# Optimization experiments

Measured on AMD Instinct MI355X. Metric: run time of the kernel, lower is better.

The kernel has to match this reference:

```python
import jax, jax.numpy as jnp
import numpy as np

B, T, C, H = 8, 2048, 1024, 64

def setup_inputs() -> dict:
    key = jax.random.key(0)
    kx, kq, kk, kv = jax.random.split(key, 4)
    scale = 1.0 / np.sqrt(C)
    return {
        "x": jax.random.normal(kx, (B, T, C), dtype=jnp.float32),
        "Wq": jax.random.normal(kq, (C, H), dtype=jnp.float32) * scale,
        "Wk": jax.random.normal(kk, (C, H), dtype=jnp.float32) * scale,
        "Wv": jax.random.normal(kv, (C, H), dtype=jnp.float32) * scale,
    }

def reference(x, Wq, Wk, Wv):
    # q,k,v: [B,T,H]
    q = jnp.einsum('btc,ch->bth', x, Wq)
    k = jnp.einsum('btc,ch->bth', x, Wk)
    v = jnp.einsum('btc,ch->bth', x, Wv)
    scale = k.shape[-1] ** -0.5
    wei = jnp.einsum('bth,bsh->bts', q, k) * scale  # [B,T,T]
    causal = jnp.tril(jnp.ones((x.shape[1], x.shape[1]), dtype=bool))
    wei = jnp.where(causal, wei, -jnp.inf)
    wei = jax.nn.softmax(wei, axis=-1)
    out = jnp.einsum('bts,bsh->bth', wei, v)  # [B,T,H]
    return out
```

## Files before the change

### kernel.cpp

```cpp
#include <hip/hip_runtime.h>

#define B_ 8
#define T_ 2048
#define C_ 1024
#define H_ 64

typedef __bf16 bf16x8 __attribute__((ext_vector_type(8)));
typedef float  f32x4  __attribute__((ext_vector_type(4)));
typedef unsigned short u16x8 __attribute__((ext_vector_type(8)));

__device__ __forceinline__ unsigned short f2bf(float f) {
    unsigned u = __builtin_bit_cast(unsigned, f);
    u += 0x8000u;
    return (unsigned short)(u >> 16);
}

__device__ __forceinline__ float bf2f(unsigned short v) {
    unsigned u = ((unsigned)v) << 16;
    return __builtin_bit_cast(float, u);
}

__device__ __forceinline__ unsigned pack2(float lo, float hi) {
    unsigned a = __builtin_bit_cast(unsigned, lo) + 0x8000u;
    unsigned b = __builtin_bit_cast(unsigned, hi) + 0x8000u;
    return (a >> 16) | (b & 0xffff0000u);
}

union U8 { unsigned u32[4]; u16x8 v; };

__device__ __forceinline__ u16x8 cvt8(float4 f0, float4 f1) {
    U8 r;
    r.u32[0] = pack2(f0.x, f0.y);
    r.u32[1] = pack2(f0.z, f0.w);
    r.u32[2] = pack2(f1.x, f1.y);
    r.u32[3] = pack2(f1.z, f1.w);
    return r.v;
}

__device__ __forceinline__ bf16x8 load8_bf(const unsigned short* p) {
    return __builtin_bit_cast(bf16x8, *(const u16x8*)p);
}

__device__ __forceinline__ void gload_lds16(const float* g, float* l) {
    __builtin_amdgcn_global_load_lds(
        (const __attribute__((address_space(1))) unsigned int*)g,
        (__attribute__((address_space(3))) unsigned int*)l, 16, 0, 0);
}


__global__ void cast_weights(const float* __restrict__ Wq,
                             const float* __restrict__ Wk,
                             const float* __restrict__ Wv,
                             unsigned short* __restrict__ Wtf) {
    int idx = blockIdx.x * blockDim.x + threadIdx.x;
    int n   = idx % 192;
    int c   = idx / 192;
    int w   = n >> 6;
    int h   = n & 63;
    const float* W = (w == 0) ? Wq : (w == 1) ? Wk : Wv;
    int nt = n >> 4, l16 = n & 15;
    int kk = c >> 5, quad = (c >> 3) & 3, j = c & 7;
    Wtf[(size_t)(nt * 32 + kk) * 512 + l16 * 32 + quad * 8 + j] =
        f2bf(W[(size_t)c * H_ + h]);
}

__global__ __launch_bounds__(256, 2) void qkv_proj(
        const float* __restrict__ x,
        const unsigned short* __restrict__ Wtf,
        unsigned short* __restrict__ Qf,
        unsigned short* __restrict__ Kf,
        unsigned short* __restrict__ Vf) {
    __shared__ __attribute__((aligned(16))) float Axs[16 * 1024];

    const int tid  = threadIdx.x;
    const int ns   = tid >> 6;
    const int lane = tid & 63;
    const int l16  = lane & 15;
    const int quad = lane >> 4;
    const size_t r0 = (size_t)blockIdx.x * 16;
    const int bb     = (int)(r0 >> 11);
    const int tloc0  = (int)(r0 & (T_ - 1));
    const int t16_0  = tloc0 >> 4;
    const int s32    = tloc0 >> 5;
    const int half16 = t16_0 & 1;

#pragma unroll
    for (int jj = 0; jj < 16; jj++) {
        int j   = ns * 16 + jj;
        int row = j >> 2;
        int S0  = (j & 3) * 64;
        int g   = (S0 + lane) ^ (row & 7);
        const float* gp = x + (r0 + row) * C_ + g * 4;
        float* lp = &Axs[row * 1024 + S0 * 4];
        gload_lds16(gp, lp);
    }

    f32x4 acc[3];
#pragma unroll
    for (int i = 0; i < 3; i++) acc[i] = (f32x4){0.f, 0.f, 0.f, 0.f};

    const int xsw = l16 & 7;
    const unsigned short* wp = Wtf + (size_t)(ns * 3 * 32) * 512
                               + l16 * 32 + quad * 8;
    const float* Arow = &Axs[l16 * 1024];

    __syncthreads();

#pragma unroll 4
    for (int kk = 0; kk < 32; kk++) {
        int g0 = kk * 8 + quad * 2;
        float4 f0 = *(const float4*)(Arow + (size_t)((g0    ) ^ xsw) * 4);
        float4 f1 = *(const float4*)(Arow + (size_t)((g0 + 1) ^ xsw) * 4);
        bf16x8 a0 = __builtin_bit_cast(bf16x8, cvt8(f0, f1));
#pragma unroll
        for (int i = 0; i < 3; i++) {
            bf16x8 b = load8_bf(wp + (size_t)(i * 32 + kk) * 512);
            acc[i] = __builtin_amdgcn_mfma_f32_16x16x32_bf16(a0, b, acc[i], 0, 0, 0);
        }
    }

    __syncthreads();
    unsigned short* E = (unsigned short*)Axs;
#pragma unroll
    for (int i = 0; i < 3; i++) {
        int nt = ns * 3 + i;
#pragma unroll
        for (int r = 0; r < 4; r++) {
            unsigned short bv = f2bf(acc[i][r]);
            int off;
            if (nt < 4) {
                off = (nt >> 1) * 512 + (quad * 4 + r) * 32 +
                      ((nt & 1) * 2 + (l16 >> 3)) * 8 + (l16 & 7);
            } else if (nt < 8) {
                int nk = nt - 4;
                off = 1024 + (nk >> 1) * 512 + (quad * 4 + r) * 32 +
                      ((nk & 1) * 2 + (l16 >> 3)) * 8 + (l16 & 7);
            } else {
                int ht = nt - 8;
                off = 2048 + ht * 256 + l16 * 16 + quad * 4 + r;
            }
            E[off] = bv;
        }
    }
    __syncthreads();

    {
        int ch = tid >> 6;
        int g  = tid & 63;
        unsigned short* dst = (ch < 2) ? Qf : Kf;
        int part = ch & 1;
        dst += ((size_t)(bb * 128 + t16_0) * 2 + part) * 512;
        *(u16x8*)(dst + g * 8) = *(const u16x8*)(&E[ch * 512 + g * 8]);
    }
    if (tid < 128) {
        int ht   = tid >> 5;
        int rr   = tid & 31;
        int l16v = rr >> 1;
        int hh   = rr & 1;
        unsigned short* dst = Vf + ((size_t)(bb * 64 + s32) * 4 + ht) * 512
                              + l16v * 32 + half16 * 16 + hh * 8;
        *(u16x8*)dst = *(const u16x8*)(&E[2048 + ht * 256 + l16v * 16 + hh * 8]);
    }
}

#define PROW 33
#define OMS2 66

__global__ __launch_bounds__(256) void attn(
        const unsigned short* __restrict__ Qf,
        const unsigned short* __restrict__ Kf,
        const unsigned short* __restrict__ Vf,
        float* __restrict__ out) {
    __shared__ unsigned int ps_[4 * 32 * PROW];
    __shared__ unsigned short Om_[4 * 32 * OMS2];
    __shared__ float mred_[4][32];
    __shared__ float lred_[4][32];

    const int tid  = threadIdx.x;
    const int wave = tid >> 6;
    const int lane = tid & 63;
    const int l16  = lane & 15;
    const int quad = lane >> 4;
    const int b    = blockIdx.x & 7;
    const int qt32 = blockIdx.x >> 3;
    const int q0   = qt32 * 32;
    const int tdiag = qt32 >> 1;

    const int loff = l16 * 32 + quad * 8;

    bf16x8 qf[2][2];
#pragma unroll
    for (int qg = 0; qg < 2; qg++) {
        const unsigned short* Qfb = Qf + (size_t)((b * 128 + qt32 * 2 + qg) * 2) * 512;
        qf[qg][0] = load8_bf(Qfb + loff);
        qf[qg][1] = load8_bf(Qfb + 512 + loff);
    }

    f32x4 o[8];
#pragma unroll
    for (int i = 0; i < 8; i++) o[i] = (f32x4){0.f, 0.f, 0.f, 0.f};
    float m_run[2] = {-1e30f, -1e30f}, l_run[2] = {0.f, 0.f};

    const float scale = 0.125f;
    const unsigned short* Kfb = Kf + (size_t)b * 128 * 1024;
    const unsigned short* Vfb = Vf + (size_t)b * 64 * 2048;
    unsigned int* Pw = &ps_[wave * 32 * PROW];

    for (int t = wave; t <= tdiag; t += 4) {
        bf16x8 vf[8];
#pragma unroll
        for (int ks = 0; ks < 2; ks++)
#pragma unroll
            for (int ht = 0; ht < 4; ht++)
                vf[ht * 2 + ks] = load8_bf(
                    Vfb + ((size_t)(t * 2 + ks) * 4 + ht) * 512 + loff);

        f32x4 s[2][4];
#pragma unroll
        for (int nt = 0; nt < 4; nt++) {
            const unsigned short* kp = Kfb + (size_t)(t * 4 + nt) * 1024;
            bf16x8 kf0 = load8_bf(kp + loff);
            bf16x8 kf1 = load8_bf(kp + 512 + loff);
#pragma unroll
            for (int qg = 0; qg < 2; qg++) {
                f32x4 z = (f32x4){0.f, 0.f, 0.f, 0.f};
                z = __builtin_amdgcn_mfma_f32_16x16x32_bf16(kf0, qf[qg][0], z, 0, 0, 0);
                z = __builtin_amdgcn_mfma_f32_16x16x32_bf16(kf1, qf[qg][1], z, 0, 0, 0);
                s[qg][nt] = z;
            }
        }

#pragma unroll
        for (int qg = 0; qg < 2; qg++)
#pragma unroll
            for (int nt = 0; nt < 4; nt++)
#pragma unroll
                for (int r = 0; r < 4; r++) s[qg][nt][r] *= scale;

        if (t == tdiag) {
#pragma unroll
            for (int qg = 0; qg < 2; qg++) {
                int q = q0 + qg * 16 + l16;
#pragma unroll
                for (int nt = 0; nt < 4; nt++)
#pragma unroll
                    for (int r = 0; r < 4; r++) {
                        int key = t * 64 + nt * 16 + quad * 4 + r;
                        if (key > q) s[qg][nt][r] = -1e30f;
                    }
            }
        }

#pragma unroll
        for (int qg = 0; qg < 2; qg++) {
            float m0 = fmaxf(fmaxf(s[qg][0][0], s[qg][0][1]), fmaxf(s[qg][0][2], s[qg][0][3]));
            float m1 = fmaxf(fmaxf(s[qg][1][0], s[qg][1][1]), fmaxf(s[qg][1][2], s[qg][1][3]));
            float m2 = fmaxf(fmaxf(s[qg][2][0], s[qg][2][1]), fmaxf(s[qg][2][2], s[qg][2][3]));
            float m3 = fmaxf(fmaxf(s[qg][3][0], s[qg][3][1]), fmaxf(s[qg][3][2], s[qg][3][3]));
            float mx = fmaxf(fmaxf(m0, m1), fmaxf(m2, m3));
            mx = fmaxf(mx, __shfl_xor(mx, 16));
            mx = fmaxf(mx, __shfl_xor(mx, 32));
            const float m_new = fmaxf(m_run[qg], mx);
            const float alpha = __expf(m_run[qg] - m_new);
            m_run[qg] = m_new;

            float rs = 0.f;
#pragma unroll
            for (int nt = 0; nt < 4; nt++) {
#pragma unroll
                for (int i = 0; i < 2; i++) {
                    float p0 = __expf(s[qg][nt][2 * i]     - m_new);
                    float p1 = __expf(s[qg][nt][2 * i + 1] - m_new);
                    rs += p0 + p1;
                    Pw[(qg * 16 + l16) * PROW + nt * 8 + quad * 2 + i] = pack2(p0, p1);
                }
            }
            rs += __shfl_xor(rs, 16);
            rs += __shfl_xor(rs, 32);
            l_run[qg] = l_run[qg] * alpha + rs;

#pragma unroll
            for (int ht = 0; ht < 4; ht++)
#pragma unroll
                for (int r = 0; r < 4; r++) o[qg * 4 + ht][r] *= alpha;
        }

#pragma unroll
        for (int ks = 0; ks < 2; ks++) {
#pragma unroll
            for (int qg = 0; qg < 2; qg++) {
                bf16x8 pB = __builtin_bit_cast(bf16x8,
                    *(const u16x8*)(&Pw[(qg * 16 + l16) * PROW + ks * 16 + quad * 4]));
#pragma unroll
                for (int ht = 0; ht < 4; ht++)
                    o[qg * 4 + ht] = __builtin_amdgcn_mfma_f32_16x16x32_bf16(
                        vf[ht * 2 + ks], pB, o[qg * 4 + ht], 0, 0, 0);
            }
        }
    }

#pragma unroll
    for (int qg = 0; qg < 2; qg++) {
#pragma unroll
        for (int ht = 0; ht < 4; ht++)
#pragma unroll
            for (int r = 0; r < 4; r++)
                Om_[(wave * 32 + qg * 16 + l16) * OMS2 + ht * 16 + quad * 4 + r] =
                    f2bf(o[qg * 4 + ht][r]);
        if (quad == 0) {
            mred_[wave][qg * 16 + l16] = m_run[qg];
            lred_[wave][qg * 16 + l16] = l_run[qg];
        }
    }
    __syncthreads();

    const int hcol = tid & 63;
    const int qr0  = tid >> 6;
#pragma unroll
    for (int qq = 0; qq < 8; qq++) {
        const int q = qr0 + qq * 4;
        float M = -1e30f;
#pragma unroll
        for (int w = 0; w < 4; w++) M = fmaxf(M, mred_[w][q]);
        float lt = 0.f, ov = 0.f;
#pragma unroll
        for (int w = 0; w < 4; w++) {
            float e = __expf(mred_[w][q] - M);
            lt += e * lred_[w][q];
            ov += e * bf2f(Om_[(w * 32 + q) * OMS2 + hcol]);
        }
        out[((size_t)b * T_ + q0 + q) * H_ + hcol] = ov / lt;
    }
}

extern "C" void kernel_launch(void* const* d_in, const int* in_sizes, int n_in,
                              void* d_out, int out_size, void* d_ws, size_t ws_size,
                              hipStream_t stream) {
    const float* x  = (const float*)d_in[0];
    const float* Wq = (const float*)d_in[1];
    const float* Wk = (const float*)d_in[2];
    const float* Wv = (const float*)d_in[3];
    float* out = (float*)d_out;

    unsigned short* Qf  = (unsigned short*)d_ws;
    unsigned short* Kf  = Qf + (size_t)B_ * T_ * H_;
    unsigned short* Vf  = Kf + (size_t)B_ * T_ * H_;
    unsigned short* Wtf = Vf + (size_t)B_ * T_ * H_;

    cast_weights<<<(192 * C_) / 256, 256, 0, stream>>>(Wq, Wk, Wv, Wtf);
    qkv_proj<<<B_ * T_ / 16, 256, 0, stream>>>(x, Wtf, Qf, Kf, Vf);
    attn<<<B_ * (T_ / 32), 256, 0, stream>>>(Qf, Kf, Vf, out);
}
```

Measured before the change: 138.1 us.

## Make qkv_proj persistent over four row tiles with double-buffered LDS staging

Each qkv_proj block now processes 64 rows as four 16-row tiles, double-buffering the x tile in LDS. The next tile's async global-to-LDS loads are issued mid-way through the current tile's MFMA loop, so load latency overlaps compute instead of being exposed once per block. The block count drops fourfold and LDS use roughly doubles, so occupancy falls to one block per CU. That reduces the parallelism available to hide latency, and the grid of 256 blocks is small.

```diff
diff --git a/kernel.cpp b/kernel.cpp
--- a/kernel.cpp
+++ b/kernel.cpp
@@ -45,6 +45,21 @@
     __builtin_amdgcn_global_load_lds(
         (const __attribute__((address_space(1))) unsigned int*)g,
         (__attribute__((address_space(3))) unsigned int*)l, 16, 0, 0);
+}
+
+__device__ __forceinline__ void stage_rows(const float* __restrict__ x,
+                                           float* lbuf, size_t rbase,
+                                           int ns, int lane, int half) {
+#pragma unroll
+    for (int q = 0; q < 8; q++) {
+        int jj  = half * 8 + q;
+        int j   = ns * 16 + jj;
+        int row = j >> 2;
+        int S0  = (j & 3) * 64;
+        int g   = (S0 + lane) ^ (row & 7);
+        gload_lds16(x + (rbase + row) * C_ + (size_t)g * 4,
+                    lbuf + row * 1024 + S0 * 4);
+    }
 }
 
 
@@ -64,102 +79,105 @@
         f2bf(W[(size_t)c * H_ + h]);
 }
 
-__global__ __launch_bounds__(256, 2) void qkv_proj(
+__global__ __launch_bounds__(256, 1) void qkv_proj(
         const float* __restrict__ x,
         const unsigned short* __restrict__ Wtf,
         unsigned short* __restrict__ Qf,
         unsigned short* __restrict__ Kf,
         unsigned short* __restrict__ Vf) {
-    __shared__ __attribute__((aligned(16))) float Axs[16 * 1024];
+    __shared__ __attribute__((aligned(16))) float Axs[2][16 * 1024];
+    __shared__ __attribute__((aligned(16))) unsigned short E[3072];
 
     const int tid  = threadIdx.x;
     const int ns   = tid >> 6;
     const int lane = tid & 63;
     const int l16  = lane & 15;
     const int quad = lane >> 4;
-    const size_t r0 = (size_t)blockIdx.x * 16;
-    const int bb     = (int)(r0 >> 11);
-    const int tloc0  = (int)(r0 & (T_ - 1));
-    const int t16_0  = tloc0 >> 4;
-    const int s32    = tloc0 >> 5;
-    const int half16 = t16_0 & 1;
-
-#pragma unroll
-    for (int jj = 0; jj < 16; jj++) {
-        int j   = ns * 16 + jj;
-        int row = j >> 2;
-        int S0  = (j & 3) * 64;
-        int g   = (S0 + lane) ^ (row & 7);
-        const float* gp = x + (r0 + row) * C_ + g * 4;
-        float* lp = &Axs[row * 1024 + S0 * 4];
-        gload_lds16(gp, lp);
-    }
-
-    f32x4 acc[3];
-#pragma unroll
-    for (int i = 0; i < 3; i++) acc[i] = (f32x4){0.f, 0.f, 0.f, 0.f};
-
-    const int xsw = l16 & 7;
+    const size_t rblk = (size_t)blockIdx.x * 64;
+    const int bb   = (int)(rblk >> 11);
+    const int xsw  = l16 & 7;
     const unsigned short* wp = Wtf + (size_t)(ns * 3 * 32) * 512
                                + l16 * 32 + quad * 8;
-    const float* Arow = &Axs[l16 * 1024];
-
+
+    stage_rows(x, Axs[0], rblk, ns, lane, 0);
+    stage_rows(x, Axs[0], rblk, ns, lane, 1);
     __syncthreads();
 
-#pragma unroll 4
-    for (int kk = 0; kk < 32; kk++) {
-        int g0 = kk * 8 + quad * 2;
-        float4 f0 = *(const float4*)(Arow + (size_t)((g0    ) ^ xsw) * 4);
-        float4 f1 = *(const float4*)(Arow + (size_t)((g0 + 1) ^ xsw) * 4);
-        bf16x8 a0 = __builtin_bit_cast(bf16x8, cvt8(f0, f1));
+    for (int t = 0; t < 4; t++) {
+        const float* Arow = &Axs[t & 1][l16 * 1024];
+        float* bufN = &Axs[(t + 1) & 1][0];
+        const size_t rnext = rblk + (size_t)(t + 1) * 16;
+
+        f32x4 acc[3];
+#pragma unroll
+        for (int i = 0; i < 3; i++) acc[i] = (f32x4){0.f, 0.f, 0.f, 0.f};
+
+#pragma unroll
+        for (int kc = 0; kc < 4; kc++) {
+            if (kc == 1 && t < 3) stage_rows(x, bufN, rnext, ns, lane, 0);
+            if (kc == 2 && t < 3) stage_rows(x, bufN, rnext, ns, lane, 1);
+#pragma unroll
+            for (int k8 = 0; k8 < 8; k8++) {
+                const int kk = kc * 8 + k8;
+                int g0 = kk * 8 + quad * 2;
+                float4 f0 = *(const float4*)(Arow + (size_t)((g0    ) ^ xsw) * 4);
+                float4 f1 = *(const float4*)(Arow + (size_t)((g0 + 1) ^ xsw) * 4);
+                bf16x8 a0 = __builtin_bit_cast(bf16x8, cvt8(f0, f1));
+#pragma unroll
+                for (int i = 0; i < 3; i++) {
+                    bf16x8 b = load8_bf(wp + (size_t)(i * 32 + kk) * 512);
+                    acc[i] = __builtin_amdgcn_mfma_f32_16x16x32_bf16(a0, b, acc[i], 0, 0, 0);
+                }
+            }
+        }
+
+        __syncthreads();
+
+        const int tloc0  = (int)((rblk + (size_t)t * 16) & (T_ - 1));
+        const int t16_0  = tloc0 >> 4;
+        const int s32    = tloc0 >> 5;
+        const int half16 = t16_0 & 1;
+
 #pragma unroll
         for (int i = 0; i < 3; i++) {
-            bf16x8 b = load8_bf(wp + (size_t)(i * 32 + kk) * 512);
-            acc[i] = __builtin_amdgcn_mfma_f32_16x16x32_bf16(a0, b, acc[i], 0, 0, 0);
-        }
-    }
-
-    __syncthreads();
-    unsigned short* E = (unsigned short*)Axs;
-#pragma unroll
-    for (int i = 0; i < 3; i++) {
-        int nt = ns * 3 + i;
-#pragma unroll
-        for (int r = 0; r < 4; r++) {
-            unsigned short bv = f2bf(acc[i][r]);
-            int off;
-            if (nt < 4) {
-                off = (nt >> 1) * 512 + (quad * 4 + r) * 32 +
-                      ((nt & 1) * 2 + (l16 >> 3)) * 8 + (l16 & 7);
-            } else if (nt < 8) {
-                int nk = nt - 4;
-                off = 1024 + (nk >> 1) * 512 + (quad * 4 + r) * 32 +
-                      ((nk & 1) * 2 + (l16 >> 3)) * 8 + (l16 & 7);
-            } else {
-                int ht = nt - 8;
-                off = 2048 + ht * 256 + l16 * 16 + quad * 4 + r;
-            }
-            E[off] = bv;
-        }
-    }
-    __syncthreads();
-
-    {
-        int ch = tid >> 6;
-        int g  = tid & 63;
-        unsigned short* dst = (ch < 2) ? Qf : Kf;
-        int part = ch & 1;
-        dst += ((size_t)(bb * 128 + t16_0) * 2 + part) * 512;
-        *(u16x8*)(dst + g * 8) = *(const u16x8*)(&E[ch * 512 + g * 8]);
-    }
-    if (tid < 128) {
-        int ht   = tid >> 5;
-        int rr   = tid & 31;
-        int l16v = rr >> 1;
-        int hh   = rr & 1;
-        unsigned short* dst = Vf + ((size_t)(bb * 64 + s32) * 4 + ht) * 512
-                              + l16v * 32 + half16 * 16 + hh * 8;
-        *(u16x8*)dst = *(const u16x8*)(&E[2048 + ht * 256 + l16v * 16 + hh * 8]);
+            int nt = ns * 3 + i;
+#pragma unroll
+            for (int r = 0; r < 4; r++) {
+                unsigned short bv = f2bf(acc[i][r]);
+                int off;
+                if (nt < 4) {
+                    off = (nt >> 1) * 512 + (quad * 4 + r) * 32 +
+                          ((nt & 1) * 2 + (l16 >> 3)) * 8 + (l16 & 7);
+                } else if (nt < 8) {
+                    int nk = nt - 4;
+                    off = 1024 + (nk >> 1) * 512 + (quad * 4 + r) * 32 +
+                          ((nk & 1) * 2 + (l16 >> 3)) * 8 + (l16 & 7);
+                } else {
+                    int ht = nt - 8;
+                    off = 2048 + ht * 256 + l16 * 16 + quad * 4 + r;
+                }
+                E[off] = bv;
+            }
+        }
+        __syncthreads();
+
+        {
+            int ch = tid >> 6;
+            int g  = tid & 63;
+            unsigned short* dst = (ch < 2) ? Qf : Kf;
+            int part = ch & 1;
+            dst += ((size_t)(bb * 128 + t16_0) * 2 + part) * 512;
+            *(u16x8*)(dst + g * 8) = *(const u16x8*)(&E[ch * 512 + g * 8]);
+        }
+        if (tid < 128) {
+            int ht   = tid >> 5;
+            int rr   = tid & 31;
+            int l16v = rr >> 1;
+            int hh   = rr & 1;
+            unsigned short* dst = Vf + ((size_t)(bb * 64 + s32) * 4 + ht) * 512
+                                  + l16v * 32 + half16 * 16 + hh * 8;
+            *(u16x8*)dst = *(const u16x8*)(&E[2048 + ht * 256 + l16v * 16 + hh * 8]);
+        }
     }
 }
 
@@ -348,6 +366,6 @@
     unsigned short* Wtf = Vf + (size_t)B_ * T_ * H_;
 
     cast_weights<<<(192 * C_) / 256, 256, 0, stream>>>(Wq, Wk, Wv, Wtf);
-    qkv_proj<<<B_ * T_ / 16, 256, 0, stream>>>(x, Wtf, Qf, Kf, Vf);
+    qkv_proj<<<B_ * T_ / 64, 256, 0, stream>>>(x, Wtf, Qf, Kf, Vf);
     attn<<<B_ * (T_ / 32), 256, 0, stream>>>(Qf, Kf, Vf, out);
 }
```

Measured after the change: 149.3 us. +8.2%, slower.
